# Kernel optimization log

Hardware: AMD Instinct MI355X
Metric: run time of the kernel (lower is better)

The kernel has to match this reference:

```python
import jax, jax.numpy as jnp
import numpy as np


def setup_inputs() -> dict:
    key = jax.random.key(0)
    k1, k2 = jax.random.split(key)
    N, C, H, W = 8, 256, 96, 96
    Cw, KK = 32, 9  # groups=8 -> C_w = C/8; ks=3 -> K*K=9
    x = jax.random.normal(k1, (N, C, H, W), dtype=jnp.float32)
    w = jax.random.normal(k2, (N, Cw, KK, H, W), dtype=jnp.float32)
    return {"x": x, "w": w}


def reference(x, w):
    # x: (N, C, H, W); w: (N, C_w, K*K, H, W)
    N, C, H, W = x.shape
    Cw, KK = w.shape[1], w.shape[2]
    K = int(np.sqrt(KK))
    pad = (K - 1) // 2
    G = C // Cw
    xp = jnp.pad(x, ((0, 0), (0, 0), (pad, pad), (pad, pad)))
    out = jnp.zeros((N, G, Cw, H, W), dtype=x.dtype)
    # accumulate over the K*K taps without materializing the full window tensor;
    # window index k = a*K + b corresponds to xp[..., h+a, w+b]
    for k in range(KK):
        a, b = divmod(k, K)
        win = xp[:, :, a:a + H, b:b + W].reshape(N, G, Cw, H, W)
        out = out + win * w[:, None, :, k]
    return out.reshape(N, C, H, W)
```

## Files before the change

kernel.cpp:

```cpp
#include <hip/hip_runtime.h>


#define N_  8
#define C_  256
#define H_  96
#define W_  96
#define CW_ 32
#define G_  8

typedef float f32x4 __attribute__((ext_vector_type(4)));

__global__ __launch_bounds__(256, 4) void SKA_kernel(const float* __restrict__ x,
                                                     const float* __restrict__ wgt,
                                                     float* __restrict__ out) {
    constexpr size_t PLANE = (size_t)H_ * W_;

    const int tid   = threadIdx.x;
    const int widx  = tid & 31;
    const int rowid = tid >> 5;
    const int lane  = tid & 63;

    const int blk = blockIdx.x;
    const int ht  = blk % (H_ / 8);
    const int t1  = blk / (H_ / 8);
    const int cw  = t1 % CW_;
    const int n   = t1 / CW_;
    const int h   = ht * 8 + rowid;
    const int w0  = widx * 4;

    if (widx >= 24) return;

    const float* wb = wgt + (((size_t)(n * CW_ + cw) * 9) * H_ + (size_t)h) * W_ + w0;
    f32x4 wv[9];
#pragma unroll
    for (int k = 0; k < 9; ++k)
        wv[k] = *reinterpret_cast<const f32x4*>(wb + (size_t)k * PLANE);

    f32x4 acc[G_];
#pragma unroll
    for (int g = 0; g < G_; ++g) acc[g] = (f32x4)(0.f);

    const float* xb = x + ((size_t)n * C_ + cw) * PLANE + w0;

#pragma unroll
    for (int a = 0; a < 3; ++a) {
        const int hh = h + a - 1;
        if (hh < 0 || hh >= H_) continue;
        const f32x4 w0v = wv[a * 3 + 0];
        const f32x4 w1v = wv[a * 3 + 1];
        const f32x4 w2v = wv[a * 3 + 2];

        f32x4 xm[G_];
#pragma unroll
        for (int g = 0; g < G_; ++g)
            xm[g] = *reinterpret_cast<const f32x4*>(
                xb + (size_t)(g * CW_) * PLANE + (size_t)hh * W_);

#pragma unroll
        for (int g = 0; g < G_; ++g) {
            float xl = __shfl(xm[g].w, lane - 1);
            float xr = __shfl(xm[g].x, lane + 1);
            xl = (widx == 0) ? 0.f : xl;
            xr = (widx == 23) ? 0.f : xr;
            acc[g].x = fmaf(xl,      w0v.x, acc[g].x);
            acc[g].x = fmaf(xm[g].x, w1v.x, acc[g].x);
            acc[g].x = fmaf(xm[g].y, w2v.x, acc[g].x);
            acc[g].y = fmaf(xm[g].x, w0v.y, acc[g].y);
            acc[g].y = fmaf(xm[g].y, w1v.y, acc[g].y);
            acc[g].y = fmaf(xm[g].z, w2v.y, acc[g].y);
            acc[g].z = fmaf(xm[g].y, w0v.z, acc[g].z);
            acc[g].z = fmaf(xm[g].z, w1v.z, acc[g].z);
            acc[g].z = fmaf(xm[g].w, w2v.z, acc[g].z);
            acc[g].w = fmaf(xm[g].z, w0v.w, acc[g].w);
            acc[g].w = fmaf(xm[g].w, w1v.w, acc[g].w);
            acc[g].w = fmaf(xr,      w2v.w, acc[g].w);
        }
    }

    float* ob = out + ((size_t)n * C_ + cw) * PLANE + (size_t)h * W_ + w0;
#pragma unroll
    for (int g = 0; g < G_; ++g) {
        __builtin_nontemporal_store(
            acc[g], reinterpret_cast<f32x4*>(ob + (size_t)(g * CW_) * PLANE));
    }
}

extern "C" void kernel_launch(void* const* d_in, const int* in_sizes, int n_in,
                              void* d_out, int out_size, void* d_ws, size_t ws_size,
                              hipStream_t stream) {
    const float* x   = (const float*)d_in[0];
    const float* wgt = (const float*)d_in[1];
    float* out = (float*)d_out;

    constexpr int grid = N_ * CW_ * (H_ / 8);
    SKA_kernel<<<grid, 256, 0, stream>>>(x, wgt, out);
}
```

Measured before the change: 43.19 us.

## Software-pipeline row loads with double buffers and sched barriers

Restructures the three-row tap loop into explicit stages. Two rows of x are loaded up front into double buffers and the third row's loads are issued before the middle-row compute, with sched_barriers fixing the order. Row indices are clamped so loads are unconditional, and weight loads become nontemporal. Occupancy hint lowers from 4 to 3 blocks per CU to make room for the extra registers, which may reduce latency hiding from concurrent waves.

```diff
diff --git a/kernel.cpp b/kernel.cpp
--- a/kernel.cpp
+++ b/kernel.cpp
@@ -10,7 +10,33 @@
 
 typedef float f32x4 __attribute__((ext_vector_type(4)));
 
-__global__ __launch_bounds__(256, 4) void SKA_kernel(const float* __restrict__ x,
+#define COMPUTE(A, XM)                                                        \
+    {                                                                         \
+        const f32x4 wa = wv[(A) * 3 + 0];                                     \
+        const f32x4 wb_ = wv[(A) * 3 + 1];                                    \
+        const f32x4 wc = wv[(A) * 3 + 2];                                     \
+        _Pragma("unroll")                                                     \
+        for (int g = 0; g < G_; ++g) {                                        \
+            float xl = __shfl(XM[g].w, lane - 1);                             \
+            float xr = __shfl(XM[g].x, lane + 1);                             \
+            xl = (widx == 0) ? 0.f : xl;                                      \
+            xr = (widx == 23) ? 0.f : xr;                                     \
+            acc[g].x = fmaf(xl,       wa.x, acc[g].x);                        \
+            acc[g].x = fmaf(XM[g].x,  wb_.x, acc[g].x);                       \
+            acc[g].x = fmaf(XM[g].y,  wc.x, acc[g].x);                        \
+            acc[g].y = fmaf(XM[g].x,  wa.y, acc[g].y);                        \
+            acc[g].y = fmaf(XM[g].y,  wb_.y, acc[g].y);                       \
+            acc[g].y = fmaf(XM[g].z,  wc.y, acc[g].y);                        \
+            acc[g].z = fmaf(XM[g].y,  wa.z, acc[g].z);                        \
+            acc[g].z = fmaf(XM[g].z,  wb_.z, acc[g].z);                       \
+            acc[g].z = fmaf(XM[g].w,  wc.z, acc[g].z);                        \
+            acc[g].w = fmaf(XM[g].z,  wa.w, acc[g].w);                        \
+            acc[g].w = fmaf(XM[g].w,  wb_.w, acc[g].w);                       \
+            acc[g].w = fmaf(xr,       wc.w, acc[g].w);                        \
+        }                                                                     \
+    }
+
+__global__ __launch_bounds__(256, 3) void SKA_kernel(const float* __restrict__ x,
                                                      const float* __restrict__ wgt,
                                                      float* __restrict__ out) {
     constexpr size_t PLANE = (size_t)H_ * W_;
@@ -34,7 +60,8 @@
     f32x4 wv[9];
 #pragma unroll
     for (int k = 0; k < 9; ++k)
-        wv[k] = *reinterpret_cast<const f32x4*>(wb + (size_t)k * PLANE);
+        wv[k] = __builtin_nontemporal_load(
+            reinterpret_cast<const f32x4*>(wb + (size_t)k * PLANE));
 
     f32x4 acc[G_];
 #pragma unroll
@@ -42,40 +69,34 @@
 
     const float* xb = x + ((size_t)n * C_ + cw) * PLANE + w0;
 
-#pragma unroll
-    for (int a = 0; a < 3; ++a) {
-        const int hh = h + a - 1;
-        if (hh < 0 || hh >= H_) continue;
-        const f32x4 w0v = wv[a * 3 + 0];
-        const f32x4 w1v = wv[a * 3 + 1];
-        const f32x4 w2v = wv[a * 3 + 2];
+    const int hm1 = (h - 1 < 0) ? 0 : h - 1;
+    const int hp1 = (h + 1 >= H_) ? H_ - 1 : h + 1;
 
-        f32x4 xm[G_];
-#pragma unroll
-        for (int g = 0; g < G_; ++g)
-            xm[g] = *reinterpret_cast<const f32x4*>(
-                xb + (size_t)(g * CW_) * PLANE + (size_t)hh * W_);
+    f32x4 xmA[G_], xmB[G_];
 
 #pragma unroll
-        for (int g = 0; g < G_; ++g) {
-            float xl = __shfl(xm[g].w, lane - 1);
-            float xr = __shfl(xm[g].x, lane + 1);
-            xl = (widx == 0) ? 0.f : xl;
-            xr = (widx == 23) ? 0.f : xr;
-            acc[g].x = fmaf(xl,      w0v.x, acc[g].x);
-            acc[g].x = fmaf(xm[g].x, w1v.x, acc[g].x);
-            acc[g].x = fmaf(xm[g].y, w2v.x, acc[g].x);
-            acc[g].y = fmaf(xm[g].x, w0v.y, acc[g].y);
-            acc[g].y = fmaf(xm[g].y, w1v.y, acc[g].y);
-            acc[g].y = fmaf(xm[g].z, w2v.y, acc[g].y);
-            acc[g].z = fmaf(xm[g].y, w0v.z, acc[g].z);
-            acc[g].z = fmaf(xm[g].z, w1v.z, acc[g].z);
-            acc[g].z = fmaf(xm[g].w, w2v.z, acc[g].z);
-            acc[g].w = fmaf(xm[g].z, w0v.w, acc[g].w);
-            acc[g].w = fmaf(xm[g].w, w1v.w, acc[g].w);
-            acc[g].w = fmaf(xr,      w2v.w, acc[g].w);
-        }
-    }
+    for (int g = 0; g < G_; ++g)
+        xmA[g] = *reinterpret_cast<const f32x4*>(
+            xb + (size_t)(g * CW_) * PLANE + (size_t)hm1 * W_);
+#pragma unroll
+    for (int g = 0; g < G_; ++g)
+        xmB[g] = *reinterpret_cast<const f32x4*>(
+            xb + (size_t)(g * CW_) * PLANE + (size_t)h * W_);
+    __builtin_amdgcn_sched_barrier(0);
+
+    if (h > 0) COMPUTE(0, xmA)
+    __builtin_amdgcn_sched_barrier(0);
+
+#pragma unroll
+    for (int g = 0; g < G_; ++g)
+        xmA[g] = *reinterpret_cast<const f32x4*>(
+            xb + (size_t)(g * CW_) * PLANE + (size_t)hp1 * W_);
+    __builtin_amdgcn_sched_barrier(0);
+
+    COMPUTE(1, xmB)
+    __builtin_amdgcn_sched_barrier(0);
+
+    if (h < H_ - 1) COMPUTE(2, xmA)
 
     float* ob = out + ((size_t)n * C_ + cw) * PLANE + (size_t)h * W_ + w0;
 #pragma unroll
```

Result: slower. 46.72 us (+8.2%).

## Issue all 24 x row loads up front via inline asm and remap block order for XCDs

Applied to the files above, without the earlier changes.

Loads all three input rows for all eight groups at once using inline-asm global_load_dwordx4, clamping out-of-range rows instead of skipping them, then waits once before computing. This raises memory-level parallelism per thread compared with the per-row load-then-compute loop. It also permutes block indices so consecutive blocks on the same XCD handle neighbouring tiles, which is meant to improve L2 reuse of the halo rows. The cost is many more live VGPRs (96 for x plus weights), and dropping the min-blocks launch bound may reduce occupancy.

```diff
diff --git a/kernel.cpp b/kernel.cpp
--- a/kernel.cpp
+++ b/kernel.cpp
@@ -1,4 +1,5 @@
 #include <hip/hip_runtime.h>
+#include <stdint.h>
 
 
 #define N_  8
@@ -7,81 +8,93 @@
 #define W_  96
 #define CW_ 32
 #define G_  8
+#define PL_ (H_ * W_)
 
 typedef float f32x4 __attribute__((ext_vector_type(4)));
 
-__global__ __launch_bounds__(256, 4) void SKA_kernel(const float* __restrict__ x,
-                                                     const float* __restrict__ wgt,
-                                                     float* __restrict__ out) {
-    constexpr size_t PLANE = (size_t)H_ * W_;
+#define GLD(dst, addr) \
+    asm volatile("global_load_dwordx4 %0, %1, off" : "=v"(dst) : "v"(addr))
 
+__global__ __launch_bounds__(256) void SKA_kernel(const float* __restrict__ x,
+                                                  const float* __restrict__ wgt,
+                                                  float* __restrict__ out) {
     const int tid   = threadIdx.x;
     const int widx  = tid & 31;
     const int rowid = tid >> 5;
     const int lane  = tid & 63;
 
-    const int blk = blockIdx.x;
-    const int ht  = blk % (H_ / 8);
-    const int t1  = blk / (H_ / 8);
-    const int cw  = t1 % CW_;
-    const int n   = t1 / CW_;
-    const int h   = ht * 8 + rowid;
-    const int w0  = widx * 4;
+    const int b  = blockIdx.x;
+    const int lb = (b & 7) * 384 + (b >> 3);
+    const int ht = lb % 12;
+    const int t1 = lb / 12;
+    const int cw = t1 % CW_;
+    const int n  = t1 / CW_;
+    const int h  = ht * 8 + rowid;
+    const int w0 = widx * 4;
 
     if (widx >= 24) return;
 
-    const float* wb = wgt + (((size_t)(n * CW_ + cw) * 9) * H_ + (size_t)h) * W_ + w0;
+    const float* wb = wgt + (size_t)(((n * CW_ + cw) * 9) * H_ + h) * W_ + w0;
     f32x4 wv[9];
 #pragma unroll
     for (int k = 0; k < 9; ++k)
-        wv[k] = *reinterpret_cast<const f32x4*>(wb + (size_t)k * PLANE);
+        wv[k] = *reinterpret_cast<const f32x4*>(wb + k * PL_);
+
+    const float* xb = x + (size_t)((n * C_ + cw) * PL_) + w0;
+    const int r0 = (h - 1 < 0) ? 0 : h - 1;
+    const int r2 = (h + 1 >= H_) ? H_ - 1 : h + 1;
+    const int rows[3] = {r0, h, r2};
+
+    f32x4 xm[3][G_];
+#pragma unroll
+    for (int a = 0; a < 3; ++a) {
+#pragma unroll
+        for (int g = 0; g < G_; ++g) {
+            GLD(xm[a][g], xb + (size_t)(g * CW_) * PL_ + rows[a] * W_);
+        }
+    }
+
+    asm volatile("s_waitcnt vmcnt(0)" ::: "memory");
+    __builtin_amdgcn_sched_barrier(0);
 
     f32x4 acc[G_];
 #pragma unroll
     for (int g = 0; g < G_; ++g) acc[g] = (f32x4)(0.f);
 
-    const float* xb = x + ((size_t)n * C_ + cw) * PLANE + w0;
-
 #pragma unroll
     for (int a = 0; a < 3; ++a) {
         const int hh = h + a - 1;
         if (hh < 0 || hh >= H_) continue;
-        const f32x4 w0v = wv[a * 3 + 0];
-        const f32x4 w1v = wv[a * 3 + 1];
-        const f32x4 w2v = wv[a * 3 + 2];
-
-        f32x4 xm[G_];
-#pragma unroll
-        for (int g = 0; g < G_; ++g)
-            xm[g] = *reinterpret_cast<const f32x4*>(
-                xb + (size_t)(g * CW_) * PLANE + (size_t)hh * W_);
-
+        const f32x4 wa = wv[a * 3 + 0];
+        const f32x4 wm = wv[a * 3 + 1];
+        const f32x4 wc = wv[a * 3 + 2];
 #pragma unroll
         for (int g = 0; g < G_; ++g) {
-            float xl = __shfl(xm[g].w, lane - 1);
-            float xr = __shfl(xm[g].x, lane + 1);
+            const f32x4 xv = xm[a][g];
+            float xl = __shfl(xv.w, lane - 1);
+            float xr = __shfl(xv.x, lane + 1);
             xl = (widx == 0) ? 0.f : xl;
             xr = (widx == 23) ? 0.f : xr;
-            acc[g].x = fmaf(xl,      w0v.x, acc[g].x);
-            acc[g].x = fmaf(xm[g].x, w1v.x, acc[g].x);
-            acc[g].x = fmaf(xm[g].y, w2v.x, acc[g].x);
-            acc[g].y = fmaf(xm[g].x, w0v.y, acc[g].y);
-            acc[g].y = fmaf(xm[g].y, w1v.y, acc[g].y);
-            acc[g].y = fmaf(xm[g].z, w2v.y, acc[g].y);
-            acc[g].z = fmaf(xm[g].y, w0v.z, acc[g].z);
-            acc[g].z = fmaf(xm[g].z, w1v.z, acc[g].z);
-            acc[g].z = fmaf(xm[g].w, w2v.z, acc[g].z);
-            acc[g].w = fmaf(xm[g].z, w0v.w, acc[g].w);
-            acc[g].w = fmaf(xm[g].w, w1v.w, acc[g].w);
-            acc[g].w = fmaf(xr,      w2v.w, acc[g].w);
+            acc[g].x = fmaf(xl,   wa.x, acc[g].x);
+            acc[g].x = fmaf(xv.x, wm.x, acc[g].x);
+            acc[g].x = fmaf(xv.y, wc.x, acc[g].x);
+            acc[g].y = fmaf(xv.x, wa.y, acc[g].y);
+            acc[g].y = fmaf(xv.y, wm.y, acc[g].y);
+            acc[g].y = fmaf(xv.z, wc.y, acc[g].y);
+            acc[g].z = fmaf(xv.y, wa.z, acc[g].z);
+            acc[g].z = fmaf(xv.z, wm.z, acc[g].z);
+            acc[g].z = fmaf(xv.w, wc.z, acc[g].z);
+            acc[g].w = fmaf(xv.z, wa.w, acc[g].w);
+            acc[g].w = fmaf(xv.w, wm.w, acc[g].w);
+            acc[g].w = fmaf(xr,   wc.w, acc[g].w);
         }
     }
 
-    float* ob = out + ((size_t)n * C_ + cw) * PLANE + (size_t)h * W_ + w0;
+    float* ob = out + (size_t)((n * C_ + cw) * PL_) + h * W_ + w0;
 #pragma unroll
     for (int g = 0; g < G_; ++g) {
         __builtin_nontemporal_store(
-            acc[g], reinterpret_cast<f32x4*>(ob + (size_t)(g * CW_) * PLANE));
+            acc[g], reinterpret_cast<f32x4*>(ob + (size_t)(g * CW_) * PL_));
     }
 }
 
```

Result: slower. 44.06 us (+2.0%).
